# Optimization experiments

Hardware: AMD Instinct MI355X
Metric: run time of the kernel (lower is better)

Reference implementation:

```python
import jax, jax.numpy as jnp
import numpy as np

N_NODES = 50000
N_EDGES = 200000
NODE_DIM = 32   # in_channels (== hidden_dim, required by NNConv nn output size)
EDGE_DIM = 16
HIDDEN = 32
OUT_DIM = 32
EPS = 1e-5
SLOPE = 0.01  # LeakyReLU default negative_slope


def setup_inputs() -> dict:
    key = jax.random.key(0)
    ks = jax.random.split(key, 16)
    inp = {
        "x": jax.random.normal(ks[0], (N_NODES, NODE_DIM), dtype=jnp.float32),
        "edge_index": jax.random.randint(ks[1], (2, N_EDGES), 0, N_NODES, dtype=jnp.int64),
        "edge_attr": jax.random.normal(ks[2], (N_EDGES, EDGE_DIM), dtype=jnp.float32),
        "batch": jnp.zeros((N_NODES,), dtype=jnp.int64),
        # edge MLP params
        "W1": jax.random.normal(ks[3], (EDGE_DIM, HIDDEN), dtype=jnp.float32) / np.sqrt(EDGE_DIM),
        "b1": jnp.zeros((HIDDEN,), dtype=jnp.float32),
        "bn1_gamma": jnp.ones((HIDDEN,), dtype=jnp.float32),
        "bn1_beta": jnp.zeros((HIDDEN,), dtype=jnp.float32),
        "bn1_mean": jax.random.normal(ks[4], (HIDDEN,), dtype=jnp.float32) * 0.1,
        "bn1_var": jax.random.uniform(ks[5], (HIDDEN,), dtype=jnp.float32, minval=0.5, maxval=1.5),
        "W2": jax.random.normal(ks[6], (HIDDEN, HIDDEN * OUT_DIM), dtype=jnp.float32) / np.sqrt(HIDDEN),
        "b2": jnp.zeros((HIDDEN * OUT_DIM,), dtype=jnp.float32),
        "bn2_gamma": jnp.ones((HIDDEN * OUT_DIM,), dtype=jnp.float32),
        "bn2_beta": jnp.zeros((HIDDEN * OUT_DIM,), dtype=jnp.float32),
        "bn2_mean": jax.random.normal(ks[7], (HIDDEN * OUT_DIM,), dtype=jnp.float32) * 0.1,
        "bn2_var": jax.random.uniform(ks[8], (HIDDEN * OUT_DIM,), dtype=jnp.float32, minval=0.5, maxval=1.5),
        # NNConv root weight + bias
        "root": jax.random.normal(ks[9], (NODE_DIM, OUT_DIM), dtype=jnp.float32) / np.sqrt(NODE_DIM),
        "bias": jnp.zeros((OUT_DIM,), dtype=jnp.float32),
    }
    return inp


def _leaky_relu(h):
    return jnp.where(h >= 0, h, SLOPE * h)


def _bn_eval(h, gamma, beta, mean, var):
    return (h - mean) * (gamma / jnp.sqrt(var + EPS)) + beta


def reference(x, edge_index, edge_attr, batch, W1, b1, bn1_gamma, bn1_beta, bn1_mean, bn1_var,
              W2, b2, bn2_gamma, bn2_beta, bn2_mean, bn2_var, root, bias):
    n_nodes = x.shape[0]
    # edge MLP (Dropout is identity in eval mode)
    h = edge_attr @ W1 + b1                                   # [E, H]
    h = _leaky_relu(_bn_eval(h, bn1_gamma, bn1_beta, bn1_mean, bn1_var))
    w = h @ W2 + b2                                           # [E, H*O]
    w = _leaky_relu(_bn_eval(w, bn2_gamma, bn2_beta, bn2_mean, bn2_var))
    w = w.reshape(-1, NODE_DIM, OUT_DIM)                      # [E, in, out]
    # gather source node features, per-edge bmm, scatter-add to destinations
    src, dst = edge_index[0], edge_index[1]
    x_j = x[src]                                              # [E, in]
    msg = jnp.einsum('ei,eio->eo', x_j, w)                    # [E, out]
    aggr = jax.ops.segment_sum(msg, dst, num_segments=n_nodes)
    return aggr + x @ root + bias
```

## Files before the change

kernel.cpp:

```cpp
#include <hip/hip_runtime.h>
#include <math.h>

#define ED 16
#define HD 32
#define OD 32
#define KD 1024
#define EPB 512
#define TPW 4
#define HPAD 34
#define CAP 32

typedef float  f32x4  __attribute__((ext_vector_type(4)));
typedef float  v4f    __attribute__((ext_vector_type(4)));
typedef short  bf16x8 __attribute__((ext_vector_type(8)));
typedef short  bf16x4 __attribute__((ext_vector_type(4)));

constexpr int LOFF_HX  = 0;
constexpr int LOFF_WHI = EPB * HPAD * 2;
constexpr int LOFF_W1T = LOFF_WHI + 32768;
constexpr int LOFF_B1  = LOFF_W1T + 2048;
constexpr int LOFF_BF  = LOFF_B1 + 128;
constexpr int LOFF_DST = LOFF_BF + 2048;
constexpr int LDS_TOTAL= LOFF_DST + 2048;

__device__ inline unsigned short bf16_rne(float v) {
    unsigned int u = __float_as_uint(v);
    return (unsigned short)((u + 0x7FFFu + ((u >> 16) & 1u)) >> 16);
}

__device__ __forceinline__ void stage_weights(
    int t, int s, unsigned char* smem,
    const float* __restrict__ W1, const float* __restrict__ b1,
    const float* __restrict__ g1, const float* __restrict__ be1,
    const float* __restrict__ m1, const float* __restrict__ v1,
    const float* __restrict__ W2, const float* __restrict__ b2,
    const float* __restrict__ g2, const float* __restrict__ be2,
    const float* __restrict__ m2, const float* __restrict__ v2)
{
    float* w1t = (float*)(smem + LOFF_W1T);
    float* b1s = (float*)(smem + LOFF_B1);
    float* bfL = (float*)(smem + LOFF_BF);
    unsigned short* wLhi = (unsigned short*)(smem + LOFF_WHI);

    {
        int c = t >> 4, j = t & 15;
        float sc = g1[c] / sqrtf(v1[c] + 1e-5f);
        w1t[t] = W1[j * HD + c] * sc;
    }
    if (t < HD) {
        float sc = g1[t] / sqrtf(v1[t] + 1e-5f);
        b1s[t] = b1[t] * sc + be1[t] - m1[t] * sc;
    }
    {
        int i = t >> 4, m = t & 15;
        int k = (2 * i + s) * 16 + m;
        float sc = g2[k] / sqrtf(v2[k] + 1e-5f);
        bfL[t] = b2[k] * sc + be2[k] - m2[k] * sc;
    }
#pragma unroll
    for (int p = 0; p < 4; ++p) {
        int c = t + p * 512;
        int i = c >> 6, ln = c & 63;
        int m = ln & 15, quad = ln >> 4;
        int k = (2 * i + s) * 16 + m;
        float sc = g2[k] / sqrtf(v2[k] + 1e-5f);
        bf16x8 w;
#pragma unroll
        for (int idx = 0; idx < 8; ++idx) {
            int j = quad * 8 + idx;
            w[idx] = (short)bf16_rne(W2[j * KD + k] * sc);
        }
        *(bf16x8*)(wLhi + (size_t)c * 8) = w;
    }
}

__device__ __forceinline__ void edge_tile(
    int t, int s, int tileBase, unsigned char* smem,
    const float* __restrict__ x, const int* __restrict__ eidx,
    const float* __restrict__ ea_g,
    unsigned short* __restrict__ msgb, int* __restrict__ cnt,
    int* __restrict__ bucket, int nE)
{
    unsigned short* hHi = (unsigned short*)(smem + LOFF_HX);
    unsigned short* xS  = (unsigned short*)(smem + LOFF_HX);
    const unsigned short* wLhi = (const unsigned short*)(smem + LOFF_WHI);
    const float* w1t = (const float*)(smem + LOFF_W1T);
    const float* b1s = (const float*)(smem + LOFF_B1);
    const float* bfL = (const float*)(smem + LOFF_BF);
    int* dstS = (int*)(smem + LOFF_DST);

    int e = tileBase + t;
    int ec = (e < nE) ? e : (nE - 1);
    int my_src = __builtin_nontemporal_load(eidx + ec);
    int my_dst = __builtin_nontemporal_load(eidx + nE + ec);

    const v4f* xrow_p = (const v4f*)(x + (size_t)my_src * HD);
    v4f xrow[8];
#pragma unroll
    for (int q = 0; q < 8; ++q) xrow[q] = xrow_p[q];

    const v4f* eap = (const v4f*)(ea_g + (size_t)ec * ED);
    v4f a0 = __builtin_nontemporal_load(eap + 0);
    v4f a1 = __builtin_nontemporal_load(eap + 1);
    v4f a2 = __builtin_nontemporal_load(eap + 2);
    v4f a3 = __builtin_nontemporal_load(eap + 3);

    dstS[t] = my_dst;

    float hreg[HD];
#pragma unroll
    for (int c = 0; c < HD; ++c) {
        const v4f* r4 = (const v4f*)(w1t + c * ED);
        v4f w0 = r4[0], w1 = r4[1], w2 = r4[2], w3 = r4[3];
        float acc = b1s[c];
        acc = fmaf(a0.x, w0.x, acc); acc = fmaf(a0.y, w0.y, acc);
        acc = fmaf(a0.z, w0.z, acc); acc = fmaf(a0.w, w0.w, acc);
        acc = fmaf(a1.x, w1.x, acc); acc = fmaf(a1.y, w1.y, acc);
        acc = fmaf(a1.z, w1.z, acc); acc = fmaf(a1.w, w1.w, acc);
        acc = fmaf(a2.x, w2.x, acc); acc = fmaf(a2.y, w2.y, acc);
        acc = fmaf(a2.z, w2.z, acc); acc = fmaf(a2.w, w2.w, acc);
        acc = fmaf(a3.x, w3.x, acc); acc = fmaf(a3.y, w3.y, acc);
        acc = fmaf(a3.z, w3.z, acc); acc = fmaf(a3.w, w3.w, acc);
        hreg[c] = fmaxf(acc, 0.01f * acc);
    }

#pragma unroll
    for (int ch = 0; ch < 4; ++ch) {
        bf16x8 phi;
#pragma unroll
        for (int u = 0; u < 8; ++u)
            phi[u] = (short)bf16_rne(hreg[ch * 8 + u]);
        *(bf16x8*)(hHi + t * HPAD + ch * 8) = phi;
    }
    __syncthreads();

    const int wave = t >> 6;
    const int lane = t & 63;
    const int n = lane & 15;
    const int quad = lane >> 4;
    const int ebase = wave * 64;

    bf16x8 bHi[TPW];
#pragma unroll
    for (int tt = 0; tt < TPW; ++tt) {
        int edge = ebase + tt * 16 + n;
        bHi[tt] = *(const bf16x8*)(hHi + edge * HPAD + quad * 8);
    }

    int xdst[TPW];
    bool evalid[TPW];
    int xoff[TPW];
    int geid[TPW];
#pragma unroll
    for (int tt = 0; tt < TPW; ++tt) {
        int le = ebase + tt * 16 + n;
        geid[tt] = tileBase + le;
        evalid[tt] = geid[tt] < nE;
        xdst[tt] = dstS[le];
        xoff[tt] = le * HPAD;
    }

    __syncthreads();

#pragma unroll
    for (int ch = 0; ch < 4; ++ch) {
        bf16x8 px;
#pragma unroll
        for (int u = 0; u < 8; ++u) {
            int q = ch * 2 + (u >> 2);
            px[u] = (short)bf16_rne(xrow[q][u & 3]);
        }
        *(bf16x8*)(xS + t * HPAD + ch * 8) = px;
    }
    __syncthreads();

    f32x4 msg[TPW];
#pragma unroll
    for (int tt = 0; tt < TPW; ++tt)
        msg[tt] = (f32x4){0.f, 0.f, 0.f, 0.f};

#pragma unroll 4
    for (int i = 0; i < HD; ++i) {
        const bf16x8 cH = *(const bf16x8*)(wLhi + i * 512 + lane * 8);
        const f32x4 b0 = *(const f32x4*)(bfL + i * 16 + quad * 4);
        float xv[TPW];
#pragma unroll
        for (int tt = 0; tt < TPW; ++tt) {
            unsigned int u = xS[xoff[tt] + i];
            xv[tt] = __uint_as_float(u << 16);
        }
#pragma unroll
        for (int tt = 0; tt < TPW; ++tt) {
            f32x4 c = b0;
            c = __builtin_amdgcn_mfma_f32_16x16x32_bf16(cH, bHi[tt], c, 0, 0, 0);
            f32x4 w = __builtin_elementwise_max(c, 0.01f * c);
            f32x4 xs = {xv[tt], xv[tt], xv[tt], xv[tt]};
            msg[tt] = __builtin_elementwise_fma(xs, w, msg[tt]);
        }
    }

#pragma unroll
    for (int tt = 0; tt < TPW; ++tt) {
        if (!evalid[tt]) continue;
        bf16x4 pm;
#pragma unroll
        for (int r = 0; r < 4; ++r) pm[r] = (short)bf16_rne(msg[tt][r]);
        __builtin_nontemporal_store(pm,
            (bf16x4*)(msgb + (size_t)geid[tt] * OD + s * 16 + quad * 4));
    }
    if (s == 0 && quad == 0) {
#pragma unroll
        for (int tt = 0; tt < TPW; ++tt) {
            if (!evalid[tt]) continue;
            int pos = atomicAdd(cnt + xdst[tt], 1);
            if (pos < CAP) bucket[(size_t)xdst[tt] * CAP + pos] = geid[tt];
        }
    }
}

__global__ __launch_bounds__(512, 4)
void edge_k(const float* __restrict__ x, const int* __restrict__ eidx,
            const float* __restrict__ ea,
            const float* __restrict__ W1, const float* __restrict__ b1,
            const float* __restrict__ g1, const float* __restrict__ be1,
            const float* __restrict__ m1, const float* __restrict__ v1,
            const float* __restrict__ W2, const float* __restrict__ b2,
            const float* __restrict__ g2, const float* __restrict__ be2,
            const float* __restrict__ m2, const float* __restrict__ v2,
            unsigned short* msgb, int* cnt, int* bucket, int nE)
{
    __shared__ __align__(16) unsigned char smem[LDS_TOTAL];
    const int t = threadIdx.x;
    const int s = blockIdx.y;
    stage_weights(t, s, smem, W1, b1, g1, be1, m1, v1,
                  W2, b2, g2, be2, m2, v2);
    __syncthreads();
    edge_tile(t, s, (int)blockIdx.x * EPB, smem, x, eidx, ea, msgb, cnt, bucket, nE);
}

__global__ __launch_bounds__(512)
void gather_k(const float* __restrict__ x, const float* __restrict__ root,
              const float* __restrict__ bias,
              const unsigned short* __restrict__ msgb,
              const int* __restrict__ bucket, const int* __restrict__ cnt,
              const int* __restrict__ eidx,
              float* __restrict__ out, int nN, int nE)
{
    __shared__ __align__(16) float rootS[HD * OD];
    __shared__ __align__(16) float biasS[OD];
    __shared__ float xsh[16][33];

    const int t = threadIdx.x;
    if (t < 256)      ((v4f*)rootS)[t] = ((const v4f*)root)[t];
    else if (t < 264) ((v4f*)biasS)[t - 256] = ((const v4f*)bias)[t - 256];

    const int nodeBase = blockIdx.x * 16;
    if (t < 128) {
        int nl = t >> 3, q = t & 7;
        int node = nodeBase + nl;
        if (node >= nN) node = nN - 1;
        v4f v = ((const v4f*)(x + (size_t)node * HD))[q];
        xsh[nl][4 * q + 0] = v.x;
        xsh[nl][4 * q + 1] = v.y;
        xsh[nl][4 * q + 2] = v.z;
        xsh[nl][4 * q + 3] = v.w;
    }
    __syncthreads();

    const int nl = t >> 5, ch = t & 31;
    const int v = nodeBase + nl;
    if (v >= nN) return;

    float acc = biasS[ch];
#pragma unroll
    for (int i = 0; i < HD; ++i)
        acc = fmaf(xsh[nl][i], rootS[i * OD + ch], acc);

    int c = cnt[v];
    if (c <= CAP) {
        const int* bk = bucket + (size_t)v * CAP;
        for (int p = 0; p < c; ++p) {
            int e = bk[p];
            unsigned int u = msgb[(size_t)e * OD + ch];
            acc += __uint_as_float(u << 16);
        }
    } else {
        const int* dstp = eidx + nE;
        for (int e = 0; e < nE; ++e)
            if (dstp[e] == v) {
                unsigned int u = msgb[(size_t)e * OD + ch];
                acc += __uint_as_float(u << 16);
            }
    }
    __builtin_nontemporal_store(acc, out + (size_t)v * OD + ch);
}

__global__ void root_init_k(const float* __restrict__ x, const float* __restrict__ root,
                            const float* __restrict__ bias, float* __restrict__ out, int nN)
{
    int t = blockIdx.x * blockDim.x + threadIdx.x;
    if (t >= nN * OD) return;
    int o = t & (OD - 1);
    int n = t >> 5;
    const float* xr = x + (size_t)n * HD;
    float acc = bias[o];
#pragma unroll
    for (int i = 0; i < HD; ++i)
        acc = fmaf(xr[i], root[i * OD + o], acc);
    out[t] = acc;
}

__global__ __launch_bounds__(64)
void edge_raw_k(const float* __restrict__ x, const int* __restrict__ eidx,
                const float* __restrict__ ea_g,
                const float* __restrict__ W1, const float* __restrict__ b1,
                const float* __restrict__ g1, const float* __restrict__ be1,
                const float* __restrict__ m1, const float* __restrict__ v1,
                const float* __restrict__ W2, const float* __restrict__ b2,
                const float* __restrict__ g2, const float* __restrict__ be2,
                const float* __restrict__ m2, const float* __restrict__ v2,
                float* __restrict__ out, int nE)
{
    int e = blockIdx.x * 64 + threadIdx.x;
    if (e >= nE) return;
    const int obase = blockIdx.y * 16;
    int src = eidx[e];
    int dst = eidx[nE + e];
    float eav[ED];
#pragma unroll
    for (int j = 0; j < ED; ++j) eav[j] = ea_g[(size_t)e * ED + j];
    float h[HD];
#pragma unroll
    for (int c = 0; c < HD; ++c) {
        float acc = b1[c];
#pragma unroll
        for (int j = 0; j < ED; ++j) acc = fmaf(eav[j], W1[j * HD + c], acc);
        float sc = g1[c] / sqrtf(v1[c] + 1e-5f);
        acc = (acc - m1[c]) * sc + be1[c];
        h[c] = fmaxf(acc, 0.01f * acc);
    }
    float msg[16];
#pragma unroll
    for (int o = 0; o < 16; ++o) msg[o] = 0.f;
    const float* xj = x + (size_t)src * HD;
    for (int i = 0; i < HD; ++i) {
        float xv = xj[i];
#pragma unroll
        for (int oo = 0; oo < 16; ++oo) {
            int k = i * OD + obase + oo;
            float acc = b2[k];
#pragma unroll
            for (int j = 0; j < HD; ++j) acc = fmaf(h[j], W2[j * KD + k], acc);
            float sc = g2[k] / sqrtf(v2[k] + 1e-5f);
            acc = (acc - m2[k]) * sc + be2[k];
            float w = fmaxf(acc, 0.01f * acc);
            msg[oo] = fmaf(xv, w, msg[oo]);
        }
    }
    float* op = out + (size_t)dst * OD + obase;
#pragma unroll
    for (int oo = 0; oo < 16; ++oo) atomicAdd(op + oo, msg[oo]);
}

extern "C" void kernel_launch(void* const* d_in, const int* in_sizes, int n_in,
                              void* d_out, int out_size, void* d_ws, size_t ws_size,
                              hipStream_t stream)
{
    const float* x    = (const float*)d_in[0];
    const int*   eidx = (const int*)  d_in[1];
    const float* ea   = (const float*)d_in[2];
    const float* W1   = (const float*)d_in[4];
    const float* b1   = (const float*)d_in[5];
    const float* g1   = (const float*)d_in[6];
    const float* be1  = (const float*)d_in[7];
    const float* m1   = (const float*)d_in[8];
    const float* v1   = (const float*)d_in[9];
    const float* W2   = (const float*)d_in[10];
    const float* b2   = (const float*)d_in[11];
    const float* g2   = (const float*)d_in[12];
    const float* be2  = (const float*)d_in[13];
    const float* m2   = (const float*)d_in[14];
    const float* v2   = (const float*)d_in[15];
    const float* root = (const float*)d_in[16];
    const float* bias = (const float*)d_in[17];
    float* out = (float*)d_out;

    int nN = in_sizes[0] / HD;
    int nE = in_sizes[2] / ED;

    size_t msgB = (size_t)nE * OD * 2;
    size_t OFF_BKT = (msgB + 15) & ~(size_t)15;
    size_t OFF_CNT = OFF_BKT + (size_t)nN * CAP * 4;
    size_t need = OFF_CNT + (size_t)nN * 4;

    if (ws_size >= need) {
        unsigned char* wsb = (unsigned char*)d_ws;
        unsigned short* msgb = (unsigned short*)wsb;
        int* bucket = (int*)(wsb + OFF_BKT);
        int* cnt    = (int*)(wsb + OFF_CNT);

        hipMemsetAsync(cnt, 0, (size_t)nN * 4, stream);
        int nTiles = (nE + EPB - 1) / EPB;
        edge_k<<<dim3(nTiles, 2), 512, 0, stream>>>(
            x, eidx, ea, W1, b1, g1, be1, m1, v1,
            W2, b2, g2, be2, m2, v2, msgb, cnt, bucket, nE);
        gather_k<<<(nN + 15) / 16, 512, 0, stream>>>(
            x, root, bias, msgb, bucket, cnt, eidx, out, nN, nE);
    } else {
        root_init_k<<<(nN * OD + 255) / 256, 256, 0, stream>>>(x, root, bias, out, nN);
        edge_raw_k<<<dim3((nE + 63) / 64, 2), 64, 0, stream>>>(
            x, eidx, ea, W1, b1, g1, be1, m1, v1,
            W2, b2, g2, be2, m2, v2, out, nE);
    }
}
```

Baseline: 187.6 us.

## Precompute folded edge-MLP weights once and process both output halves per block

A new prep kernel folds the batch-norm scales into W1/W2, converts W2 to bf16 in MFMA fragment layout once into workspace, and zeroes the counters, replacing the memset and the per-block recomputation from raw parameters. The edge kernel now covers 256 edges per block and computes both 16-column output halves in sequence, reloading the second W2 half from workspace. The first layer, the gather of x and edge_attr, and the bucket atomics are no longer duplicated across two grid halves. Messages are stored as one 8-element bf16 vector in a permuted column order, and the gather kernel remaps its column index to match. The cost is an extra launch, two barriers for reloading weights within each block, and less edge parallelism per block.

```diff
diff --git a/kernel.cpp b/kernel.cpp
--- a/kernel.cpp
+++ b/kernel.cpp
@@ -5,8 +5,8 @@
 #define HD 32
 #define OD 32
 #define KD 1024
-#define EPB 512
-#define TPW 4
+#define EPB 256
+#define TPW 2
 #define HPAD 34
 #define CAP 32
 
@@ -15,122 +15,162 @@
 typedef short  bf16x8 __attribute__((ext_vector_type(8)));
 typedef short  bf16x4 __attribute__((ext_vector_type(4)));
 
+constexpr size_t OFF_MSG = 72064;
+
 constexpr int LOFF_HX  = 0;
-constexpr int LOFF_WHI = EPB * HPAD * 2;
+constexpr int LOFF_WHI = 17408;
 constexpr int LOFF_W1T = LOFF_WHI + 32768;
 constexpr int LOFF_B1  = LOFF_W1T + 2048;
 constexpr int LOFF_BF  = LOFF_B1 + 128;
-constexpr int LOFF_DST = LOFF_BF + 2048;
-constexpr int LDS_TOTAL= LOFF_DST + 2048;
+constexpr int LOFF_DST = LOFF_BF + 4096;
+constexpr int LDS_TOTAL= LOFF_DST + 1024;
 
 __device__ inline unsigned short bf16_rne(float v) {
     unsigned int u = __float_as_uint(v);
     return (unsigned short)((u + 0x7FFFu + ((u >> 16) & 1u)) >> 16);
 }
 
-__device__ __forceinline__ void stage_weights(
-    int t, int s, unsigned char* smem,
-    const float* __restrict__ W1, const float* __restrict__ b1,
-    const float* __restrict__ g1, const float* __restrict__ be1,
-    const float* __restrict__ m1, const float* __restrict__ v1,
-    const float* __restrict__ W2, const float* __restrict__ b2,
-    const float* __restrict__ g2, const float* __restrict__ be2,
-    const float* __restrict__ m2, const float* __restrict__ v2)
-{
+__global__ __launch_bounds__(256)
+void prep_kernel(const float* __restrict__ W1, const float* __restrict__ b1,
+                 const float* __restrict__ g1, const float* __restrict__ be1,
+                 const float* __restrict__ m1, const float* __restrict__ v1,
+                 const float* __restrict__ W2, const float* __restrict__ b2,
+                 const float* __restrict__ g2, const float* __restrict__ be2,
+                 const float* __restrict__ m2, const float* __restrict__ v2,
+                 unsigned char* __restrict__ wsb, int* __restrict__ cnt, int nN)
+{
+    float* w1t = (float*)(wsb);
+    float* b1f = (float*)(wsb + 2048);
+    float* bf  = (float*)(wsb + 2176);
+    unsigned short* ahi = (unsigned short*)(wsb + 6272);
+
+    int bt = blockIdx.x * blockDim.x + threadIdx.x;
+    int stride = gridDim.x * blockDim.x;
+
+    for (int q = bt; q < nN; q += stride) cnt[q] = 0;
+
+    for (int q = bt; q < HD * ED; q += stride) {
+        int c = q >> 4, j = q & 15;
+        float s = g1[c] / sqrtf(v1[c] + 1e-5f);
+        w1t[q] = W1[j * HD + c] * s;
+    }
+    for (int c = bt; c < HD; c += stride) {
+        float s = g1[c] / sqrtf(v1[c] + 1e-5f);
+        b1f[c] = b1[c] * s + be1[c] - m1[c] * s;
+    }
+    for (int k = bt; k < KD; k += stride) {
+        float s = g2[k] / sqrtf(v2[k] + 1e-5f);
+        bf[k] = b2[k] * s + be2[k] - m2[k] * s;
+    }
+    for (int p = bt; p < KD * HD; p += stride) {
+        int j = p >> 10, k = p & 1023;
+        float s = g2[k] / sqrtf(v2[k] + 1e-5f);
+        float v = W2[p] * s;
+        int g = k >> 4, m = k & 15;
+        int quad = j >> 3, idx = j & 7;
+        int q = g * 512 + (quad * 16 + m) * 8 + idx;
+        ahi[q] = bf16_rne(v);
+    }
+}
+
+__global__ __launch_bounds__(512, 4)
+void edge_k(const float* __restrict__ x, const int* __restrict__ eidx,
+            const float* __restrict__ ea_g, const unsigned char* __restrict__ wsb,
+            unsigned short* __restrict__ msgb, int* __restrict__ cnt,
+            int* __restrict__ bucket, int nE)
+{
+    __shared__ __align__(16) unsigned char smem[LDS_TOTAL];
+    float*          eaS = (float*)(smem + LOFF_HX);
+    unsigned short* hHi = (unsigned short*)(smem + LOFF_HX);
+    unsigned short* xS  = (unsigned short*)(smem + LOFF_HX);
+    unsigned short* wLhi = (unsigned short*)(smem + LOFF_WHI);
     float* w1t = (float*)(smem + LOFF_W1T);
     float* b1s = (float*)(smem + LOFF_B1);
     float* bfL = (float*)(smem + LOFF_BF);
-    unsigned short* wLhi = (unsigned short*)(smem + LOFF_WHI);
-
+    int*  dstS = (int*)(smem + LOFF_DST);
+
+    const int t = threadIdx.x;
+    const int el = t & 255;
+    const int chalf = t >> 8;
+    const int tileBase = (int)blockIdx.x * EPB;
+
+    const float* wsW1 = (const float*)(wsb);
+    const float* wsB1 = (const float*)(wsb + 2048);
+    const v4f*   wsBf4 = (const v4f*)(wsb + 2176);
+    const v4f*   srcHi = (const v4f*)(wsb + 6272);
+
+    int e = tileBase + el;
+    int ec = (e < nE) ? e : (nE - 1);
+    v4f xrow[8];
+    if (chalf == 0) {
+        int my_src = __builtin_nontemporal_load(eidx + ec);
+        dstS[el] = __builtin_nontemporal_load(eidx + nE + ec);
+        const v4f* xrow_p = (const v4f*)(x + (size_t)my_src * HD);
+#pragma unroll
+        for (int q = 0; q < 8; ++q) xrow[q] = xrow_p[q];
+        const v4f* eap = (const v4f*)(ea_g + (size_t)ec * ED);
+        v4f a0 = __builtin_nontemporal_load(eap + 0);
+        v4f a1 = __builtin_nontemporal_load(eap + 1);
+        v4f a2 = __builtin_nontemporal_load(eap + 2);
+        v4f a3 = __builtin_nontemporal_load(eap + 3);
+        float* er = eaS + el * 17;
+        er[0]=a0.x; er[1]=a0.y; er[2]=a0.z; er[3]=a0.w;
+        er[4]=a1.x; er[5]=a1.y; er[6]=a1.z; er[7]=a1.w;
+        er[8]=a2.x; er[9]=a2.y; er[10]=a2.z; er[11]=a2.w;
+        er[12]=a3.x; er[13]=a3.y; er[14]=a3.z; er[15]=a3.w;
+    }
+
+    if (t < 256) {
+        int d = t & 127, sh = t >> 7;
+        ((v4f*)bfL)[sh * 128 + d] = wsBf4[(d >> 2) * 8 + sh * 4 + (d & 3)];
+    } else if (t < 384) {
+        ((v4f*)w1t)[t - 256] = ((const v4f*)wsW1)[t - 256];
+    } else if (t < 392) {
+        ((v4f*)b1s)[t - 384] = ((const v4f*)wsB1)[t - 384];
+    }
     {
-        int c = t >> 4, j = t & 15;
-        float sc = g1[c] / sqrtf(v1[c] + 1e-5f);
-        w1t[t] = W1[j * HD + c] * sc;
-    }
-    if (t < HD) {
-        float sc = g1[t] / sqrtf(v1[t] + 1e-5f);
-        b1s[t] = b1[t] * sc + be1[t] - m1[t] * sc;
-    }
-    {
-        int i = t >> 4, m = t & 15;
-        int k = (2 * i + s) * 16 + m;
-        float sc = g2[k] / sqrtf(v2[k] + 1e-5f);
-        bfL[t] = b2[k] * sc + be2[k] - m2[k] * sc;
-    }
-#pragma unroll
-    for (int p = 0; p < 4; ++p) {
-        int c = t + p * 512;
-        int i = c >> 6, ln = c & 63;
-        int m = ln & 15, quad = ln >> 4;
-        int k = (2 * i + s) * 16 + m;
-        float sc = g2[k] / sqrtf(v2[k] + 1e-5f);
-        bf16x8 w;
-#pragma unroll
-        for (int idx = 0; idx < 8; ++idx) {
-            int j = quad * 8 + idx;
-            w[idx] = (short)bf16_rne(W2[j * KD + k] * sc);
-        }
-        *(bf16x8*)(wLhi + (size_t)c * 8) = w;
-    }
-}
-
-__device__ __forceinline__ void edge_tile(
-    int t, int s, int tileBase, unsigned char* smem,
-    const float* __restrict__ x, const int* __restrict__ eidx,
-    const float* __restrict__ ea_g,
-    unsigned short* __restrict__ msgb, int* __restrict__ cnt,
-    int* __restrict__ bucket, int nE)
-{
-    unsigned short* hHi = (unsigned short*)(smem + LOFF_HX);
-    unsigned short* xS  = (unsigned short*)(smem + LOFF_HX);
-    const unsigned short* wLhi = (const unsigned short*)(smem + LOFF_WHI);
-    const float* w1t = (const float*)(smem + LOFF_W1T);
-    const float* b1s = (const float*)(smem + LOFF_B1);
-    const float* bfL = (const float*)(smem + LOFF_BF);
-    int* dstS = (int*)(smem + LOFF_DST);
-
-    int e = tileBase + t;
-    int ec = (e < nE) ? e : (nE - 1);
-    int my_src = __builtin_nontemporal_load(eidx + ec);
-    int my_dst = __builtin_nontemporal_load(eidx + nE + ec);
-
-    const v4f* xrow_p = (const v4f*)(x + (size_t)my_src * HD);
-    v4f xrow[8];
-#pragma unroll
-    for (int q = 0; q < 8; ++q) xrow[q] = xrow_p[q];
-
-    const v4f* eap = (const v4f*)(ea_g + (size_t)ec * ED);
-    v4f a0 = __builtin_nontemporal_load(eap + 0);
-    v4f a1 = __builtin_nontemporal_load(eap + 1);
-    v4f a2 = __builtin_nontemporal_load(eap + 2);
-    v4f a3 = __builtin_nontemporal_load(eap + 3);
-
-    dstS[t] = my_dst;
-
-    float hreg[HD];
-#pragma unroll
-    for (int c = 0; c < HD; ++c) {
+        v4f* dstHi = (v4f*)wLhi;
+#pragma unroll
+        for (int p = 0; p < 4; ++p) {
+            int c = t + p * 512;
+            int sc = (2 * (c >> 6) + 0) * 64 + (c & 63);
+            dstHi[c] = srcHi[sc];
+        }
+    }
+    __syncthreads();
+
+    const float* eaR = eaS + el * 17;
+    float ea0 = eaR[0], ea1 = eaR[1], ea2 = eaR[2], ea3 = eaR[3];
+    float ea4 = eaR[4], ea5 = eaR[5], ea6 = eaR[6], ea7 = eaR[7];
+    float ea8 = eaR[8], ea9 = eaR[9], ea10 = eaR[10], ea11 = eaR[11];
+    float ea12 = eaR[12], ea13 = eaR[13], ea14 = eaR[14], ea15 = eaR[15];
+    const int c0 = chalf * 16;
+    float hreg[16];
+#pragma unroll
+    for (int cc = 0; cc < 16; ++cc) {
+        const int c = c0 + cc;
         const v4f* r4 = (const v4f*)(w1t + c * ED);
         v4f w0 = r4[0], w1 = r4[1], w2 = r4[2], w3 = r4[3];
         float acc = b1s[c];
-        acc = fmaf(a0.x, w0.x, acc); acc = fmaf(a0.y, w0.y, acc);
-        acc = fmaf(a0.z, w0.z, acc); acc = fmaf(a0.w, w0.w, acc);
-        acc = fmaf(a1.x, w1.x, acc); acc = fmaf(a1.y, w1.y, acc);
-        acc = fmaf(a1.z, w1.z, acc); acc = fmaf(a1.w, w1.w, acc);
-        acc = fmaf(a2.x, w2.x, acc); acc = fmaf(a2.y, w2.y, acc);
-        acc = fmaf(a2.z, w2.z, acc); acc = fmaf(a2.w, w2.w, acc);
-        acc = fmaf(a3.x, w3.x, acc); acc = fmaf(a3.y, w3.y, acc);
-        acc = fmaf(a3.z, w3.z, acc); acc = fmaf(a3.w, w3.w, acc);
-        hreg[c] = fmaxf(acc, 0.01f * acc);
-    }
-
-#pragma unroll
-    for (int ch = 0; ch < 4; ++ch) {
+        acc = fmaf(ea0,  w0.x, acc); acc = fmaf(ea1,  w0.y, acc);
+        acc = fmaf(ea2,  w0.z, acc); acc = fmaf(ea3,  w0.w, acc);
+        acc = fmaf(ea4,  w1.x, acc); acc = fmaf(ea5,  w1.y, acc);
+        acc = fmaf(ea6,  w1.z, acc); acc = fmaf(ea7,  w1.w, acc);
+        acc = fmaf(ea8,  w2.x, acc); acc = fmaf(ea9,  w2.y, acc);
+        acc = fmaf(ea10, w2.z, acc); acc = fmaf(ea11, w2.w, acc);
+        acc = fmaf(ea12, w3.x, acc); acc = fmaf(ea13, w3.y, acc);
+        acc = fmaf(ea14, w3.z, acc); acc = fmaf(ea15, w3.w, acc);
+        hreg[cc] = fmaxf(acc, 0.01f * acc);
+    }
+    __syncthreads();
+
+#pragma unroll
+    for (int ch = 0; ch < 2; ++ch) {
         bf16x8 phi;
 #pragma unroll
         for (int u = 0; u < 8; ++u)
             phi[u] = (short)bf16_rne(hreg[ch * 8 + u]);
-        *(bf16x8*)(hHi + t * HPAD + ch * 8) = phi;
+        *(bf16x8*)(hHi + el * HPAD + c0 + ch * 8) = phi;
     }
     __syncthreads();
 
@@ -138,47 +178,38 @@
     const int lane = t & 63;
     const int n = lane & 15;
     const int quad = lane >> 4;
-    const int ebase = wave * 64;
+    const int ebase = wave * 32;
 
     bf16x8 bHi[TPW];
-#pragma unroll
-    for (int tt = 0; tt < TPW; ++tt) {
-        int edge = ebase + tt * 16 + n;
-        bHi[tt] = *(const bf16x8*)(hHi + edge * HPAD + quad * 8);
-    }
-
-    int xdst[TPW];
-    bool evalid[TPW];
-    int xoff[TPW];
-    int geid[TPW];
+    int xdst[TPW]; bool evalid[TPW]; int xoff[TPW]; int geid[TPW];
 #pragma unroll
     for (int tt = 0; tt < TPW; ++tt) {
         int le = ebase + tt * 16 + n;
+        bHi[tt] = *(const bf16x8*)(hHi + le * HPAD + quad * 8);
         geid[tt] = tileBase + le;
         evalid[tt] = geid[tt] < nE;
         xdst[tt] = dstS[le];
         xoff[tt] = le * HPAD;
     }
-
-    __syncthreads();
-
-#pragma unroll
-    for (int ch = 0; ch < 4; ++ch) {
-        bf16x8 px;
-#pragma unroll
-        for (int u = 0; u < 8; ++u) {
-            int q = ch * 2 + (u >> 2);
-            px[u] = (short)bf16_rne(xrow[q][u & 3]);
-        }
-        *(bf16x8*)(xS + t * HPAD + ch * 8) = px;
+    __syncthreads();
+
+    if (chalf == 0) {
+#pragma unroll
+        for (int ch = 0; ch < 4; ++ch) {
+            bf16x8 px;
+#pragma unroll
+            for (int u = 0; u < 8; ++u) {
+                int q = ch * 2 + (u >> 2);
+                px[u] = (short)bf16_rne(xrow[q][u & 3]);
+            }
+            *(bf16x8*)(xS + el * HPAD + ch * 8) = px;
+        }
     }
     __syncthreads();
 
     f32x4 msg[TPW];
 #pragma unroll
-    for (int tt = 0; tt < TPW; ++tt)
-        msg[tt] = (f32x4){0.f, 0.f, 0.f, 0.f};
-
+    for (int tt = 0; tt < TPW; ++tt) msg[tt] = (f32x4){0.f, 0.f, 0.f, 0.f};
 #pragma unroll 4
     for (int i = 0; i < HD; ++i) {
         const bf16x8 cH = *(const bf16x8*)(wLhi + i * 512 + lane * 8);
@@ -198,17 +229,14 @@
             msg[tt] = __builtin_elementwise_fma(xs, w, msg[tt]);
         }
     }
-
+    bf16x4 pm0[TPW];
 #pragma unroll
     for (int tt = 0; tt < TPW; ++tt) {
-        if (!evalid[tt]) continue;
-        bf16x4 pm;
-#pragma unroll
-        for (int r = 0; r < 4; ++r) pm[r] = (short)bf16_rne(msg[tt][r]);
-        __builtin_nontemporal_store(pm,
-            (bf16x4*)(msgb + (size_t)geid[tt] * OD + s * 16 + quad * 4));
-    }
-    if (s == 0 && quad == 0) {
+#pragma unroll
+        for (int r = 0; r < 4; ++r) pm0[tt][r] = (short)bf16_rne(msg[tt][r]);
+    }
+
+    if (quad == 0) {
 #pragma unroll
         for (int tt = 0; tt < TPW; ++tt) {
             if (!evalid[tt]) continue;
@@ -216,26 +244,53 @@
             if (pos < CAP) bucket[(size_t)xdst[tt] * CAP + pos] = geid[tt];
         }
     }
-}
-
-__global__ __launch_bounds__(512, 4)
-void edge_k(const float* __restrict__ x, const int* __restrict__ eidx,
-            const float* __restrict__ ea,
-            const float* __restrict__ W1, const float* __restrict__ b1,
-            const float* __restrict__ g1, const float* __restrict__ be1,
-            const float* __restrict__ m1, const float* __restrict__ v1,
-            const float* __restrict__ W2, const float* __restrict__ b2,
-            const float* __restrict__ g2, const float* __restrict__ be2,
-            const float* __restrict__ m2, const float* __restrict__ v2,
-            unsigned short* msgb, int* cnt, int* bucket, int nE)
-{
-    __shared__ __align__(16) unsigned char smem[LDS_TOTAL];
-    const int t = threadIdx.x;
-    const int s = blockIdx.y;
-    stage_weights(t, s, smem, W1, b1, g1, be1, m1, v1,
-                  W2, b2, g2, be2, m2, v2);
-    __syncthreads();
-    edge_tile(t, s, (int)blockIdx.x * EPB, smem, x, eidx, ea, msgb, cnt, bucket, nE);
+
+    __syncthreads();
+    {
+        v4f* dstHi = (v4f*)wLhi;
+#pragma unroll
+        for (int p = 0; p < 4; ++p) {
+            int c = t + p * 512;
+            int sc = (2 * (c >> 6) + 1) * 64 + (c & 63);
+            dstHi[c] = srcHi[sc];
+        }
+    }
+    __syncthreads();
+
+#pragma unroll
+    for (int tt = 0; tt < TPW; ++tt) msg[tt] = (f32x4){0.f, 0.f, 0.f, 0.f};
+#pragma unroll 4
+    for (int i = 0; i < HD; ++i) {
+        const bf16x8 cH = *(const bf16x8*)(wLhi + i * 512 + lane * 8);
+        const f32x4 b0 = *(const f32x4*)(bfL + 512 + i * 16 + quad * 4);
+        float xv[TPW];
+#pragma unroll
+        for (int tt = 0; tt < TPW; ++tt) {
+            unsigned int u = xS[xoff[tt] + i];
+            xv[tt] = __uint_as_float(u << 16);
+        }
+#pragma unroll
+        for (int tt = 0; tt < TPW; ++tt) {
+            f32x4 c = b0;
+            c = __builtin_amdgcn_mfma_f32_16x16x32_bf16(cH, bHi[tt], c, 0, 0, 0);
+            f32x4 w = __builtin_elementwise_max(c, 0.01f * c);
+            f32x4 xs = {xv[tt], xv[tt], xv[tt], xv[tt]};
+            msg[tt] = __builtin_elementwise_fma(xs, w, msg[tt]);
+        }
+    }
+
+#pragma unroll
+    for (int tt = 0; tt < TPW; ++tt) {
+        if (!evalid[tt]) continue;
+        bf16x8 pm;
+#pragma unroll
+        for (int r = 0; r < 4; ++r) {
+            pm[r]     = pm0[tt][r];
+            pm[4 + r] = (short)bf16_rne(msg[tt][r]);
+        }
+        __builtin_nontemporal_store(pm,
+            (bf16x8*)(msgb + (size_t)geid[tt] * OD + quad * 8));
+    }
 }
 
 __global__ __launch_bounds__(512)
@@ -271,6 +326,8 @@
     const int v = nodeBase + nl;
     if (v >= nN) return;
 
+    const int b = (((ch >> 2) & 3) << 3) + ((ch >> 4) << 2) + (ch & 3);
+
     float acc = biasS[ch];
 #pragma unroll
     for (int i = 0; i < HD; ++i)
@@ -281,14 +338,14 @@
         const int* bk = bucket + (size_t)v * CAP;
         for (int p = 0; p < c; ++p) {
             int e = bk[p];
-            unsigned int u = msgb[(size_t)e * OD + ch];
+            unsigned int u = msgb[(size_t)e * OD + b];
             acc += __uint_as_float(u << 16);
         }
     } else {
         const int* dstp = eidx + nE;
         for (int e = 0; e < nE; ++e)
             if (dstp[e] == v) {
-                unsigned int u = msgb[(size_t)e * OD + ch];
+                unsigned int u = msgb[(size_t)e * OD + b];
                 acc += __uint_as_float(u << 16);
             }
     }
@@ -389,21 +446,21 @@
     int nE = in_sizes[2] / ED;
 
     size_t msgB = (size_t)nE * OD * 2;
-    size_t OFF_BKT = (msgB + 15) & ~(size_t)15;
+    size_t OFF_BKT = (OFF_MSG + msgB + 15) & ~(size_t)15;
     size_t OFF_CNT = OFF_BKT + (size_t)nN * CAP * 4;
     size_t need = OFF_CNT + (size_t)nN * 4;
 
     if (ws_size >= need) {
         unsigned char* wsb = (unsigned char*)d_ws;
-        unsigned short* msgb = (unsigned short*)wsb;
+        unsigned short* msgb = (unsigned short*)(wsb + OFF_MSG);
         int* bucket = (int*)(wsb + OFF_BKT);
         int* cnt    = (int*)(wsb + OFF_CNT);
 
-        hipMemsetAsync(cnt, 0, (size_t)nN * 4, stream);
+        prep_kernel<<<128, 256, 0, stream>>>(
+            W1, b1, g1, be1, m1, v1, W2, b2, g2, be2, m2, v2, wsb, cnt, nN);
         int nTiles = (nE + EPB - 1) / EPB;
-        edge_k<<<dim3(nTiles, 2), 512, 0, stream>>>(
-            x, eidx, ea, W1, b1, g1, be1, m1, v1,
-            W2, b2, g2, be2, m2, v2, msgb, cnt, bucket, nE);
+        edge_k<<<dim3(nTiles), 512, 0, stream>>>(
+            x, eidx, ea, wsb, msgb, cnt, bucket, nE);
         gather_k<<<(nN + 15) / 16, 512, 0, stream>>>(
             x, root, bias, msgb, bucket, cnt, eidx, out, nN, nE);
     } else {
```

Result: faster. 172.6 us, median of 2 (-8.0%).
